# Kernel optimization log

Hardware: AMD Instinct MI355X
Metric: run time of the kernel (lower is better)

## Reference

```python
import jax, jax.numpy as jnp
import numpy as np
import math

SCALES = (1, 2, 4, 8)


def interp1d(x, L_out):
    """F.interpolate(mode='linear', align_corners=False) along last axis."""
    L_in = x.shape[-1]
    if L_in == L_out:
        return x
    scale = L_in / L_out
    src = (jnp.arange(L_out, dtype=jnp.float32) + 0.5) * scale - 0.5
    src = jnp.clip(src, 0.0, float(L_in - 1))
    i0 = jnp.floor(src).astype(jnp.int32)
    i1 = jnp.minimum(i0 + 1, L_in - 1)
    w1 = (src - i0.astype(jnp.float32)).astype(x.dtype)
    return x[..., i0] * (1.0 - w1) + x[..., i1] * w1


def setup_inputs() -> dict:
    key = jax.random.key(0)
    ks = jax.random.split(key, 5)
    B, H, S, D = 2, 16, 1024, 64
    query = jax.random.normal(ks[0], (B, H, S, D), jnp.float32)
    k = jax.random.normal(ks[1], (B, H, S, D), jnp.float32)
    v = jax.random.normal(ks[2], (B, H, S, D), jnp.float32)
    # 4 per-scale Linear(head_dim, head_dim): W[i] is [out, in] (torch layout), b[i] is [out]
    W = jax.random.normal(ks[3], (len(SCALES), D, D), jnp.float32) * (1.0 / np.sqrt(D))
    b = jax.random.normal(ks[4], (len(SCALES), D), jnp.float32) * 0.01
    return {"query": query, "key": k, "value": v, "W": W, "b": b}


def reference(query, key, value, W, b):
    B, H, S, D = query.shape
    inv_sqrt_d = 1.0 / math.sqrt(D)
    outs, probs_all = [], []
    for i, s in enumerate(SCALES):
        if s > 1:
            # avg_pool1d(kernel=stride=s) over the sequence axis
            pk = key.reshape(B, H, S // s, s, D).mean(axis=3)
            pv = value.reshape(B, H, S // s, s, D).mean(axis=3)
        else:
            pk, pv = key, value
        # per-scale linear projection of pooled keys (torch Linear: x @ W.T + b)
        proj = jnp.einsum('bhkd,ed->bhke', pk, W[i]) + b[i]
        scores = jnp.einsum('bhqd,bhkd->bhqk', query, proj) * inv_sqrt_d
        probs = jax.nn.softmax(scores, axis=-1)  # [B,H,S,S//s]
        if s > 1:
            # upsample attn probs along key axis, and pooled values along seq axis
            probs = interp1d(probs, S)                               # [B,H,S,S]
            pv = jnp.swapaxes(interp1d(jnp.swapaxes(pv, -1, -2), S), -1, -2)  # [B,H,S,D]
        outs.append(jnp.einsum('bhqk,bhkd->bhqd', probs, pv))
        probs_all.append(probs)
    combined_output = jnp.stack(outs).mean(axis=0)
    combined_attention = jnp.stack(probs_all).mean(axis=0)
    return combined_output, combined_attention
```

## Files before the change

kernel.cpp:

```cpp
#include <hip/hip_runtime.h>

#define S_LEN 1024
#define DH 64
#define NBH 32
#define CROWS 1920
#define HEAD_K (CROWS * DH)
#define NCHUNK (HEAD_K / 8)
#define ATTN_OFF (NBH * S_LEN * DH)
#define PSTR 1928

typedef __attribute__((ext_vector_type(8))) short bf8_t;
typedef __attribute__((ext_vector_type(4))) float f32x4_t;

__device__ __forceinline__ unsigned short f2bf(float x) {
  unsigned u = __float_as_uint(x);
  u += 0x7fffu + ((u >> 16) & 1u);
  return (unsigned short)(u >> 16);
}
__device__ __forceinline__ float bf2f(unsigned short h) {
  return __uint_as_float(((unsigned)h) << 16);
}

template<int SI>
__device__ __forceinline__ void prep_body(
    const float* __restrict__ key, const float* __restrict__ value,
    const float* __restrict__ W, const float* __restrict__ b,
    unsigned short* __restrict__ projB, unsigned short* __restrict__ mpvB,
    const int bh, const int jt, const int t,
    float* __restrict__ pkK, float* __restrict__ pkV, float* __restrict__ coefs)
{
  constexpr int   s    = 1 << SI;
  constexpr int   L    = 1024 >> SI;
  constexpr int   off  = (SI == 0) ? 0 : (SI == 1) ? 1024 : (SI == 2) ? 1536 : 1792;
  constexpr float invs = 1.0f / (float)s;
  const int j0 = jt << 6;

  const float* Kp = key + bh * (S_LEN * DH);
  const float* Vp = value + bh * (S_LEN * DH);

  #pragma unroll
  for (int it = 0; it < 4; it++) {
    const int i = it * 256 + t;
    const int j = i >> 4, d4 = (i & 15) << 2;
    const float* src = Kp + (j0 + j) * s * DH + d4;
    float4 a = {0.f, 0.f, 0.f, 0.f};
    #pragma unroll
    for (int f = 0; f < s; f++) {
      const float4 kv = *(const float4*)(src + f * DH);
      a.x += kv.x; a.y += kv.y; a.z += kv.z; a.w += kv.w;
    }
    a.x *= invs; a.y *= invs; a.z *= invs; a.w *= invs;
    *(float4*)&pkK[j * 68 + d4] = a;
  }

  #pragma unroll
  for (int it = 0; it < 5; it++) {
    const int i = it * 256 + t;
    if (i < 1088) {
      const int hj = i >> 4, d4 = (i & 15) << 2;
      const int jg = min(max(j0 - 2 + hj, 0), L - 1);
      const float* src = Vp + jg * s * DH + d4;
      float4 a = {0.f, 0.f, 0.f, 0.f};
      #pragma unroll
      for (int f = 0; f < s; f++) {
        const float4 vv = *(const float4*)(src + f * DH);
        a.x += vv.x; a.y += vv.y; a.z += vv.z; a.w += vv.w;
      }
      a.x *= invs; a.y *= invs; a.z *= invs; a.w *= invs;
      *(float4*)&pkV[hj * 68 + d4] = a;
    }
  }

  if (t < 64) {
    const int j = j0 + t;
    float cm = 0.f, cc = 0.f, cp = 0.f;
    const int klo = max(0, (j - 1) * s);
    const int khi = min(S_LEN - 1, (j + 2) * s);
    for (int kf = klo; kf <= khi; kf++) {
      float srcp = ((float)kf + 0.5f) * invs - 0.5f;
      srcp = fminf(fmaxf(srcp, 0.f), (float)(L - 1));
      const int i0 = (int)floorf(srcp);
      const int i1 = min(i0 + 1, L - 1);
      const float w = srcp - (float)i0;
      float u = 0.f;
      if (i0 == j) u += 1.f - w;
      if (i1 == j) u += w;
      if (u != 0.f) {
        const float g0 = u * (1.f - w), g1 = u * w;
        if (i0 == j) cc += g0; else cm += g0;
        if (i1 == j) cc += g1; else cp += g1;
      }
    }
    coefs[t * 4 + 0] = cm; coefs[t * 4 + 1] = cc; coefs[t * 4 + 2] = cp;
  }
  __syncthreads();

  {
    const int j  = t & 63;
    const int e0 = __builtin_amdgcn_readfirstlane((t >> 6) << 4);
    const float* Wp = W + SI * 4096;
    float acc[16];
    #pragma unroll
    for (int ee = 0; ee < 16; ee++) acc[ee] = b[SI * 64 + e0 + ee];
    #pragma unroll
    for (int dq = 0; dq < 16; dq++) {
      const float4 p4 = *(const float4*)&pkK[j * 68 + dq * 4];
      #pragma unroll
      for (int ee = 0; ee < 16; ee++) {
        const float4 w4 = *(const float4*)&Wp[(e0 + ee) * 64 + dq * 4];
        acc[ee] += p4.x * w4.x + p4.y * w4.y + p4.z * w4.z + p4.w * w4.w;
      }
    }
    const int ktg0 = (off + j0) >> 4;
    const int ktl  = j >> 4;
    #pragma unroll
    for (int h = 0; h < 2; h++) {
      const int e0p = e0 + h * 8;
      const int ln  = (((e0p >> 3) & 3) << 4) | (j & 15);
      bf8_t v;
      #pragma unroll
      for (int jj = 0; jj < 8; jj++) v[jj] = (short)f2bf(acc[h * 8 + jj]);
      ((bf8_t*)projB)[bh * NCHUNK + ((ktg0 + ktl) * 2 + (e0p >> 5)) * 64 + ln] = v;
    }
  }

  const int kbg0 = (off + j0) >> 5;
  #pragma unroll
  for (int cc2 = 0; cc2 < 2; cc2++) {
    const int c   = cc2 * 256 + t;
    const int kbl = c >> 8;
    const int nt  = (c >> 6) & 3;
    const int ln  = c & 63;
    const int d   = nt * 16 + (ln & 15);
    const int r0  = kbl * 32 + ((ln >> 4) & 3) * 8;
    bf8_t v;
    #pragma unroll
    for (int jj = 0; jj < 8; jj++) {
      const int rl = r0 + jj;
      const float val = coefs[rl * 4 + 0] * pkV[(rl + 1) * 68 + d] +
                        coefs[rl * 4 + 1] * pkV[(rl + 2) * 68 + d] +
                        coefs[rl * 4 + 2] * pkV[(rl + 3) * 68 + d];
      v[jj] = (short)f2bf(val);
    }
    ((bf8_t*)mpvB)[bh * NCHUNK + ((kbg0 + kbl) * 4 + nt) * 64 + ln] = v;
  }
}

__global__ __launch_bounds__(256, 4) void prep_kernel(
    const float* __restrict__ key, const float* __restrict__ value,
    const float* __restrict__ W, const float* __restrict__ b,
    unsigned short* __restrict__ projB, unsigned short* __restrict__ mpvB)
{
  __shared__ __align__(16) float pkK[64 * 68];
  __shared__ __align__(16) float pkV[68 * 68];
  __shared__ float coefs[64 * 4];
  const int t = threadIdx.x;
  const int bid = blockIdx.x;
  const int bh = bid / 30;
  const int tt = bid % 30;
  if (tt < 16)
    prep_body<0>(key, value, W, b, projB, mpvB, bh, tt, t, pkK, pkV, coefs);
  else if (tt < 24)
    prep_body<1>(key, value, W, b, projB, mpvB, bh, tt - 16, t, pkK, pkV, coefs);
  else if (tt < 28)
    prep_body<2>(key, value, W, b, projB, mpvB, bh, tt - 24, t, pkK, pkV, coefs);
  else
    prep_body<3>(key, value, W, b, projB, mpvB, bh, tt - 28, t, pkK, pkV, coefs);
}

__global__ __launch_bounds__(256, 2) void fused_attn_kernel(
    const float* __restrict__ query, const unsigned short* __restrict__ projB,
    const unsigned short* __restrict__ mpvB, float* __restrict__ out)
{
  __shared__ __align__(16) unsigned short prbf[16 * PSTR];
  const int t    = threadIdx.x;
  const int bh   = blockIdx.x & 31;
  const int qt   = blockIdx.x >> 5;
  const int q0   = qt << 4;
  const int wave = t >> 6;
  const int lane = t & 63;
  const int quad = lane >> 4;
  const int n16  = lane & 15;

  bf8_t af0, af1;
  {
    const float* qrow = query + bh * (S_LEN * DH) + (q0 + n16) * DH;
    const float4 a0 = *(const float4*)(qrow + quad * 8);
    const float4 a1 = *(const float4*)(qrow + quad * 8 + 4);
    const float4 a2 = *(const float4*)(qrow + 32 + quad * 8);
    const float4 a3 = *(const float4*)(qrow + 32 + quad * 8 + 4);
    af0[0] = (short)f2bf(a0.x); af0[1] = (short)f2bf(a0.y);
    af0[2] = (short)f2bf(a0.z); af0[3] = (short)f2bf(a0.w);
    af0[4] = (short)f2bf(a1.x); af0[5] = (short)f2bf(a1.y);
    af0[6] = (short)f2bf(a1.z); af0[7] = (short)f2bf(a1.w);
    af1[0] = (short)f2bf(a2.x); af1[1] = (short)f2bf(a2.y);
    af1[2] = (short)f2bf(a2.z); af1[3] = (short)f2bf(a2.w);
    af1[4] = (short)f2bf(a3.x); af1[5] = (short)f2bf(a3.y);
    af1[6] = (short)f2bf(a3.z); af1[7] = (short)f2bf(a3.w);
  }

  {
    const bf8_t* pB = (const bf8_t*)projB + bh * NCHUNK;
    for (int kt = wave; kt < 120; kt += 4) {
      const bf8_t b0 = pB[(kt * 2 + 0) * 64 + lane];
      const bf8_t b1 = pB[(kt * 2 + 1) * 64 + lane];
      f32x4_t c = {0.f, 0.f, 0.f, 0.f};
      c = __builtin_amdgcn_mfma_f32_16x16x32_bf16(af0, b0, c, 0, 0, 0);
      c = __builtin_amdgcn_mfma_f32_16x16x32_bf16(af1, b1, c, 0, 0, 0);
      const int col = kt * 16 + n16;
      #pragma unroll
      for (int i = 0; i < 4; i++)
        prbf[(quad * 4 + i) * PSTR + col] = f2bf(c[i] * 0.125f);
    }
  }
  __syncthreads();

  {
    const int rr = t >> 4;
    const int g  = t & 15;
    unsigned short* prr = prbf + rr * PSTR;
    #pragma unroll
    for (int si = 0; si < 4; si++) {
      const int L   = 1024 >> si;
      const int off = (si == 0) ? 0 : (si == 1) ? 1024 : (si == 2) ? 1536 : 1792;
      const int nch = L >> 2;
      float m = -1e30f;
      for (int ch = g; ch < nch; ch += 16) {
        const ushort4 u = *(const ushort4*)(prr + off + ch * 4);
        m = fmaxf(m, fmaxf(fmaxf(bf2f(u.x), bf2f(u.y)),
                           fmaxf(bf2f(u.z), bf2f(u.w))));
      }
      #pragma unroll
      for (int dlt = 8; dlt >= 1; dlt >>= 1) m = fmaxf(m, __shfl_xor(m, dlt));
      float ssum = 0.f;
      for (int ch = g; ch < nch; ch += 16) {
        ushort4 u = *(const ushort4*)(prr + off + ch * 4);
        const float e0 = __expf(bf2f(u.x) - m);
        const float e1 = __expf(bf2f(u.y) - m);
        const float e2 = __expf(bf2f(u.z) - m);
        const float e3 = __expf(bf2f(u.w) - m);
        ssum += (e0 + e1) + (e2 + e3);
        u.x = f2bf(e0); u.y = f2bf(e1); u.z = f2bf(e2); u.w = f2bf(e3);
        *(ushort4*)(prr + off + ch * 4) = u;
      }
      #pragma unroll
      for (int dlt = 8; dlt >= 1; dlt >>= 1) ssum += __shfl_xor(ssum, dlt);
      const float inv = 1.0f / ssum;
      for (int ch = g; ch < nch; ch += 16) {
        ushort4 u = *(const ushort4*)(prr + off + ch * 4);
        u.x = f2bf(bf2f(u.x) * inv); u.y = f2bf(bf2f(u.y) * inv);
        u.z = f2bf(bf2f(u.z) * inv); u.w = f2bf(bf2f(u.w) * inv);
        *(ushort4*)(prr + off + ch * 4) = u;
      }
    }
  }
  __syncthreads();

  {
    const bf8_t* pM = (const bf8_t*)mpvB + bh * NCHUNK;
    f32x4_t acc = {0.f, 0.f, 0.f, 0.f};
    for (int kb = 0; kb < 60; kb++) {
      const bf8_t a = *(const bf8_t*)(prbf + n16 * PSTR + kb * 32 + quad * 8);
      const bf8_t bb = pM[(kb * 4 + wave) * 64 + lane];
      acc = __builtin_amdgcn_mfma_f32_16x16x32_bf16(a, bb, acc, 0, 0, 0);
    }
    float* ob = out + bh * (S_LEN * DH) + q0 * DH;
    #pragma unroll
    for (int i = 0; i < 4; i++)
      ob[(quad * 4 + i) * DH + wave * 16 + n16] = acc[i] * 0.25f;
  }

  float* ab = out + ATTN_OFF + (size_t)bh * (S_LEN * S_LEN) + (size_t)q0 * S_LEN;
  for (int rep = 0; rep < 16; rep++) {
    const int idx = rep * 256 + t;
    const int rr  = idx >> 8;
    const int k0  = (idx & 255) << 2;
    const unsigned short* p2 = prbf + rr * PSTR;
    const ushort4 bs = *(const ushort4*)(p2 + k0);
    float res[4] = {bf2f(bs.x), bf2f(bs.y), bf2f(bs.z), bf2f(bs.w)};
    #pragma unroll
    for (int si = 1; si < 4; si++) {
      const int   L     = 1024 >> si;
      const int   off2  = (si == 1) ? 1024 : (si == 2) ? 1536 : 1792;
      const float inv_s = (si == 1) ? 0.5f : (si == 2) ? 0.25f : 0.125f;
      #pragma unroll
      for (int kk = 0; kk < 4; kk++) {
        float srcp = ((float)(k0 + kk) + 0.5f) * inv_s - 0.5f;
        srcp = fminf(fmaxf(srcp, 0.f), (float)(L - 1));
        const int i0 = (int)floorf(srcp);
        const int i1 = min(i0 + 1, L - 1);
        const float w = srcp - (float)i0;
        res[kk] += (1.f - w) * bf2f(p2[off2 + i0]) + w * bf2f(p2[off2 + i1]);
      }
    }
    *(float4*)(ab + (size_t)idx * 4) =
        make_float4(res[0] * 0.25f, res[1] * 0.25f,
                    res[2] * 0.25f, res[3] * 0.25f);
  }
}

extern "C" void kernel_launch(void* const* d_in, const int* in_sizes, int n_in,
                              void* d_out, int out_size, void* d_ws, size_t ws_size,
                              hipStream_t stream) {
  (void)in_sizes; (void)n_in; (void)out_size; (void)ws_size;
  const float* query = (const float*)d_in[0];
  const float* key   = (const float*)d_in[1];
  const float* value = (const float*)d_in[2];
  const float* W     = (const float*)d_in[3];
  const float* b     = (const float*)d_in[4];
  float* out = (float*)d_out;

  unsigned short* projB = (unsigned short*)d_ws;
  unsigned short* mpvB  = projB + (size_t)NBH * HEAD_K;

  prep_kernel<<<NBH * 30, 256, 0, stream>>>(key, value, W, b, projB, mpvB);
  fused_attn_kernel<<<NBH * 64, 256, 0, stream>>>(query, projB, mpvB, out);
}
```

Before: 307.8 us.

## Remap blocks per XCD, software-prefetch MFMA operands, use nontemporal output stores

Changes the block-to-(head, query tile) mapping so that blocks landing on the same XCD (block id mod 8) handle the same four heads, which should improve L2 reuse of the projected keys and pooled values. Adds register double-buffering of the global B-operand loads in both MFMA loops so the next tile's load is issued before the current MFMA. Switches the output and attention-map writes to nontemporal stores to avoid polluting cache with the large write-only stream. These raise register pressure and assume the hardware scheduler places blocks round-robin across XCDs.

```diff
diff --git a/kernel.cpp b/kernel.cpp
--- a/kernel.cpp
+++ b/kernel.cpp
@@ -174,8 +174,11 @@
 {
   __shared__ __align__(16) unsigned short prbf[16 * PSTR];
   const int t    = threadIdx.x;
-  const int bh   = blockIdx.x & 31;
-  const int qt   = blockIdx.x >> 5;
+  const int bid  = blockIdx.x;
+  const int xcd  = bid & 7;
+  const int slot = bid >> 3;
+  const int bh   = xcd * 4 + (slot >> 6);
+  const int qt   = slot & 63;
   const int q0   = qt << 4;
   const int wave = t >> 6;
   const int lane = t & 63;
@@ -201,16 +204,20 @@
 
   {
     const bf8_t* pB = (const bf8_t*)projB + bh * NCHUNK;
+    bf8_t pb0 = pB[(wave * 2 + 0) * 64 + lane];
+    bf8_t pb1 = pB[(wave * 2 + 1) * 64 + lane];
     for (int kt = wave; kt < 120; kt += 4) {
-      const bf8_t b0 = pB[(kt * 2 + 0) * 64 + lane];
-      const bf8_t b1 = pB[(kt * 2 + 1) * 64 + lane];
+      const int ktn = min(kt + 4, 119);
+      const bf8_t nb0 = pB[(ktn * 2 + 0) * 64 + lane];
+      const bf8_t nb1 = pB[(ktn * 2 + 1) * 64 + lane];
       f32x4_t c = {0.f, 0.f, 0.f, 0.f};
-      c = __builtin_amdgcn_mfma_f32_16x16x32_bf16(af0, b0, c, 0, 0, 0);
-      c = __builtin_amdgcn_mfma_f32_16x16x32_bf16(af1, b1, c, 0, 0, 0);
+      c = __builtin_amdgcn_mfma_f32_16x16x32_bf16(af0, pb0, c, 0, 0, 0);
+      c = __builtin_amdgcn_mfma_f32_16x16x32_bf16(af1, pb1, c, 0, 0, 0);
       const int col = kt * 16 + n16;
       #pragma unroll
       for (int i = 0; i < 4; i++)
         prbf[(quad * 4 + i) * PSTR + col] = f2bf(c[i] * 0.125f);
+      pb0 = nb0; pb1 = nb1;
     }
   }
   __syncthreads();
@@ -259,15 +266,20 @@
   {
     const bf8_t* pM = (const bf8_t*)mpvB + bh * NCHUNK;
     f32x4_t acc = {0.f, 0.f, 0.f, 0.f};
+    bf8_t bb0 = pM[(0 * 4 + wave) * 64 + lane];
+    bf8_t bb1 = pM[(1 * 4 + wave) * 64 + lane];
     for (int kb = 0; kb < 60; kb++) {
+      const int kbn = min(kb + 2, 59);
+      const bf8_t bbn = pM[(kbn * 4 + wave) * 64 + lane];
       const bf8_t a = *(const bf8_t*)(prbf + n16 * PSTR + kb * 32 + quad * 8);
-      const bf8_t bb = pM[(kb * 4 + wave) * 64 + lane];
-      acc = __builtin_amdgcn_mfma_f32_16x16x32_bf16(a, bb, acc, 0, 0, 0);
+      acc = __builtin_amdgcn_mfma_f32_16x16x32_bf16(a, bb0, acc, 0, 0, 0);
+      bb0 = bb1; bb1 = bbn;
     }
     float* ob = out + bh * (S_LEN * DH) + q0 * DH;
     #pragma unroll
     for (int i = 0; i < 4; i++)
-      ob[(quad * 4 + i) * DH + wave * 16 + n16] = acc[i] * 0.25f;
+      __builtin_nontemporal_store(acc[i] * 0.25f,
+                                  &ob[(quad * 4 + i) * DH + wave * 16 + n16]);
   }
 
   float* ab = out + ATTN_OFF + (size_t)bh * (S_LEN * S_LEN) + (size_t)q0 * S_LEN;
@@ -293,9 +305,10 @@
         res[kk] += (1.f - w) * bf2f(p2[off2 + i0]) + w * bf2f(p2[off2 + i1]);
       }
     }
-    *(float4*)(ab + (size_t)idx * 4) =
-        make_float4(res[0] * 0.25f, res[1] * 0.25f,
-                    res[2] * 0.25f, res[3] * 0.25f);
+    f32x4_t o4;
+    o4[0] = res[0] * 0.25f; o4[1] = res[1] * 0.25f;
+    o4[2] = res[2] * 0.25f; o4[3] = res[3] * 0.25f;
+    __builtin_nontemporal_store(o4, (f32x4_t*)(ab + (size_t)idx * 4));
   }
 }
 
```

Result: faster. 294.9 us (-4.2%).
